# Kernel optimization log

Hardware: AMD Instinct MI355X
Metric: run time of the kernel (lower is better)

## Reference

```python
import jax, jax.numpy as jnp
import numpy as np

EMB, QK, V, H = 1024, 64, 64, 16
B, S = 4, 2048


def setup_inputs() -> dict:
    key = jax.random.key(0)
    ks = jax.random.split(key, 8)
    sc = 0.02
    x_q = jax.random.normal(ks[0], (B, S, EMB), jnp.float32)
    x_k_v = jax.random.normal(ks[1], (B, S, EMB), jnp.float32)
    # causal mask: True means masked (matches torch masked_fill)
    causal = ~jnp.tril(jnp.ones((S, S), dtype=bool))
    attn_mask = jnp.broadcast_to(causal, (B, S, S))
    w_q = jax.random.normal(ks[2], (H * QK, EMB), jnp.float32) * sc
    b_q = jnp.zeros((H * QK,), jnp.float32)
    w_k = jax.random.normal(ks[3], (H * QK, EMB), jnp.float32) * sc
    b_k = jnp.zeros((H * QK,), jnp.float32)
    w_v = jax.random.normal(ks[4], (H * V, EMB), jnp.float32) * sc
    b_v = jnp.zeros((H * V,), jnp.float32)
    return {"x_q": x_q, "x_k_v": x_k_v, "attn_mask": attn_mask,
            "w_q": w_q, "b_q": b_q, "w_k": w_k, "b_k": b_k, "w_v": w_v, "b_v": b_v}


def reference(x_q, x_k_v, attn_mask, w_q, b_q, w_k, b_k, w_v, b_v):
    Bq, Sq, _ = x_q.shape
    Skv = x_k_v.shape[1]
    q = (x_q @ w_q.T + b_q).reshape(Bq, Sq, H, QK).transpose(0, 2, 1, 3)   # [B,H,Sq,QK]
    k = (x_k_v @ w_k.T + b_k).reshape(Bq, Skv, H, QK).transpose(0, 2, 1, 3)  # [B,H,Skv,QK]
    v = (x_k_v @ w_v.T + b_v).reshape(Bq, Skv, H, V).transpose(0, 2, 1, 3)   # [B,H,Skv,V]
    attn = jnp.einsum('bhqd,bhkd->bhqk', q, k) / jnp.sqrt(jnp.float32(QK))
    attn = jnp.where(attn_mask[:, None, :, :], jnp.float32(-1e9), attn)
    attn = jax.nn.softmax(attn, axis=-1)
    z = jnp.einsum('bhqk,bhkv->bhqv', attn, v)        # [B,H,Sq,V]
    z = z.transpose(0, 2, 1, 3).reshape(Bq, Sq, H * V)
    return z
```

## Files before the change

### kernel.cpp

```cpp
#include <hip/hip_runtime.h>

#define B_    4
#define H_    16
#define S_    2048
#define EMB_  1024
#define D_    64

typedef __attribute__((ext_vector_type(4))) float f32x4;
typedef __attribute__((ext_vector_type(8))) short frag_ab;
typedef unsigned short ushort_t;

__device__ __forceinline__ unsigned short f2bf(float f) {
    unsigned int u = __float_as_uint(f);
    unsigned int r = u + 0x7fffu + ((u >> 16) & 1u);
    return (unsigned short)(r >> 16);
}
__device__ __forceinline__ unsigned short f2bf_fast(float f) {
    return (unsigned short)((__float_as_uint(f) + 0x8000u) >> 16);
}

__device__ __forceinline__ void gld16(const void* g, void* l) {
    __builtin_amdgcn_global_load_lds(
        (const __attribute__((address_space(1))) void*)g,
        (__attribute__((address_space(3))) void*)l, 16, 0, 0);
}

__global__ void cvt3_kernel(const float* __restrict__ s0, const float* __restrict__ s1,
                            const float* __restrict__ s2, ushort_t* __restrict__ d0,
                            ushort_t* __restrict__ d1, ushort_t* __restrict__ d2, int n4) {
    const float* src = (blockIdx.z == 0) ? s0 : (blockIdx.z == 1 ? s1 : s2);
    ushort_t* dst = (blockIdx.z == 0) ? d0 : (blockIdx.z == 1 ? d1 : d2);
    int i = blockIdx.x * blockDim.x + threadIdx.x;
    if (i >= n4) return;
    float4 f = ((const float4*)src)[i];
    ushort4 o;
    o.x = f2bf(f.x); o.y = f2bf(f.y); o.z = f2bf(f.z); o.w = f2bf(f.w);
    ((ushort4*)dst)[i] = o;
}
__global__ void cvt2_kernel(const float* __restrict__ s0, const float* __restrict__ s1,
                            ushort_t* __restrict__ d0, ushort_t* __restrict__ d1, int n4) {
    const float* src = (blockIdx.z == 0) ? s0 : s1;
    ushort_t* dst = (blockIdx.z == 0) ? d0 : d1;
    int i = blockIdx.x * blockDim.x + threadIdx.x;
    if (i >= n4) return;
    float4 f = ((const float4*)src)[i];
    ushort4 o;
    o.x = f2bf(f.x); o.y = f2bf(f.y); o.z = f2bf(f.z); o.w = f2bf(f.w);
    ((ushort4*)dst)[i] = o;
}

__global__ __launch_bounds__(256) void vtrans_kernel(
    const ushort_t* __restrict__ v, ushort_t* __restrict__ vt) {
    const int bh = blockIdx.y;
    const int s0 = blockIdx.x * 32 + (threadIdx.x >> 6) * 8;
    const int d  = threadIdx.x & 63;
    const ushort_t* vp = v + (size_t)bh * S_ * D_;
    ushort_t tmp[8];
#pragma unroll
    for (int j = 0; j < 8; ++j) tmp[j] = vp[(size_t)(s0 + j) * D_ + d];
    *(uint4*)&vt[(size_t)bh * D_ * S_ + (size_t)d * S_ + s0] = *(const uint4*)tmp;
}

__global__ __launch_bounds__(256) void qkv_gemm(
    const ushort_t* __restrict__ xq,
    const ushort_t* __restrict__ xkv,
    const ushort_t* __restrict__ wq,
    const ushort_t* __restrict__ wk,
    const ushort_t* __restrict__ wv,
    const float* __restrict__ bq,
    const float* __restrict__ bk,
    const float* __restrict__ bv,
    ushort_t* __restrict__ qo,
    ushort_t* __restrict__ ko,
    ushort_t* __restrict__ vo)
{
    __shared__ ushort_t As[2][128 * 32];
    __shared__ ushort_t Bs[2][128 * 32];

    const int z = blockIdx.z;
    const ushort_t* A = (z == 0) ? xq : xkv;
    const ushort_t* W = (z == 0) ? wq : (z == 1 ? wk : wv);
    const float* bias = (z == 0) ? bq : (z == 1 ? bk : bv);
    ushort_t* ob = (z == 0) ? qo : (z == 1 ? ko : vo);
    const float scale = (z == 0) ? 0.125f : 1.0f;

    const int tid = threadIdx.x;
    const int m0 = blockIdx.y * 128, n0 = blockIdx.x * 128;
    const int w = tid >> 6, lane = tid & 63, quad = lane >> 4, l16 = lane & 15;
    const int wm = w & 1, wn = w >> 1;
    const int row_in = lane >> 2, c8 = (lane & 3) * 8;

    f32x4 acc[4][4];
#pragma unroll
    for (int i = 0; i < 4; ++i)
#pragma unroll
        for (int j = 0; j < 4; ++j) acc[i][j] = (f32x4){0.f, 0.f, 0.f, 0.f};

    auto stage = [&](int b, int kt) {
        const int k0 = kt * 32;
#pragma unroll
        for (int i = 0; i < 2; ++i) {
            const int base = w * 32 + i * 16;
            gld16(A + (size_t)(m0 + base + row_in) * EMB_ + k0 + c8, &As[b][base * 32]);
            gld16(W + (size_t)(n0 + base + row_in) * EMB_ + k0 + c8, &Bs[b][base * 32]);
        }
    };

    stage(0, 0);
    for (int kt = 0; kt < 32; ++kt) {
        __syncthreads();
        if (kt < 31) stage((kt + 1) & 1, kt + 1);
        const int bsel = kt & 1;

        frag_ab a[4], bfr[4];
#pragma unroll
        for (int t = 0; t < 4; ++t) {
            a[t]   = *(const frag_ab*)&As[bsel][(wm * 64 + t * 16 + l16) * 32 + quad * 8];
            bfr[t] = *(const frag_ab*)&Bs[bsel][(wn * 64 + t * 16 + l16) * 32 + quad * 8];
        }
#pragma unroll
        for (int tm = 0; tm < 4; ++tm)
#pragma unroll
            for (int tn = 0; tn < 4; ++tn)
                acc[tm][tn] = __builtin_amdgcn_mfma_f32_16x16x32_bf16(
                    a[tm], bfr[tn], acc[tm][tn], 0, 0, 0);
    }

#pragma unroll
    for (int tn = 0; tn < 4; ++tn) {
        int n = n0 + wn * 64 + tn * 16 + l16;
        float bval = bias[n];
        int hh = n >> 6, dd = n & 63;
#pragma unroll
        for (int tm = 0; tm < 4; ++tm) {
#pragma unroll
            for (int r = 0; r < 4; ++r) {
                int m = m0 + wm * 64 + tm * 16 + quad * 4 + r;
                int bb = m >> 11, ss = m & (S_ - 1);
                float val = (acc[tm][tn][r] + bval) * scale;
                ob[(((size_t)bb * H_ + hh) * S_ + ss) * D_ + dd] = f2bf(val);
            }
        }
    }
}

#define LDP 72

__global__ __launch_bounds__(256) void attn_kernel(
    const ushort_t* __restrict__ qg,
    const ushort_t* __restrict__ kg,
    const ushort_t* __restrict__ vtg,
    float* __restrict__ out)
{
    __shared__ ushort_t Kt[2][2][64 * 32];
    __shared__ ushort_t Vt[2][2][64 * 32];
    __shared__ ushort_t Pb[4][32 * LDP];

    const int tid = threadIdx.x;
    const int w = tid >> 6, lane = tid & 63, quad = lane >> 4, l16 = lane & 15;
    const int row_in = lane >> 2, c8 = (lane & 3) * 8;

    const int id = blockIdx.x;
    const int rr = id >> 3;
    const int bh = (id & 7) + 8 * (rr & 7);
    const int qi = 15 - (rr >> 3);
    const int q0 = qi * 128;
    const int b = bh >> 4, h = bh & 15;

    const ushort_t* qp  = qg  + (size_t)bh * S_ * D_;
    const ushort_t* kp  = kg  + (size_t)bh * S_ * D_;
    const ushort_t* vtp = vtg + (size_t)bh * D_ * S_;

    frag_ab aq[2][2];
#pragma unroll
    for (int rg = 0; rg < 2; ++rg) {
        const ushort_t* qr = qp + (size_t)(q0 + rg * 64 + w * 16 + l16) * D_;
        aq[rg][0] = *(const frag_ab*)(qr + quad * 8);
        aq[rg][1] = *(const frag_ab*)(qr + 32 + quad * 8);
    }

    float psum[2][4];
    f32x4 o[2][4];
#pragma unroll
    for (int rg = 0; rg < 2; ++rg)
#pragma unroll
        for (int r = 0; r < 4; ++r) { psum[rg][r] = 0.f; }
#pragma unroll
    for (int rg = 0; rg < 2; ++rg)
#pragma unroll
        for (int t = 0; t < 4; ++t) o[rg][t] = (f32x4){0.f, 0.f, 0.f, 0.f};

    ushort_t* Pw = &Pb[w][0];
    const int last = 2 * qi + 1;

    auto stage = [&](int bsel, int kt) {
        const int base = w * 16;
        const ushort_t* kgp  = kp  + (size_t)(kt * 64 + base + row_in) * D_ + c8;
        const ushort_t* vtgp = vtp + (size_t)(base + row_in) * S_ + kt * 64 + c8;
        gld16(kgp,       &Kt[bsel][0][base * 32]);
        gld16(kgp + 32,  &Kt[bsel][1][base * 32]);
        gld16(vtgp,      &Vt[bsel][0][base * 32]);
        gld16(vtgp + 32, &Vt[bsel][1][base * 32]);
    };

    stage(0, 0);
    for (int kt = 0; kt <= last; ++kt) {
        __syncthreads();
        if (kt < last) stage((kt + 1) & 1, kt + 1);
        const int bsel = kt & 1;

        frag_ab bk[4][2], bv[4][2];
#pragma unroll
        for (int t = 0; t < 4; ++t) {
#pragma unroll
            for (int hf = 0; hf < 2; ++hf) {
                bk[t][hf] = *(const frag_ab*)&Kt[bsel][hf][(t * 16 + l16) * 32 + quad * 8];
                bv[t][hf] = *(const frag_ab*)&Vt[bsel][hf][(t * 16 + l16) * 32 + quad * 8];
            }
        }

#pragma unroll
        for (int rg = 0; rg < 2; ++rg) {
            if (rg == 0 && kt == last) continue;
            f32x4 scf[4];
#pragma unroll
            for (int tn = 0; tn < 4; ++tn) {
                f32x4 sc = (f32x4){0.f, 0.f, 0.f, 0.f};
                sc = __builtin_amdgcn_mfma_f32_16x16x32_bf16(aq[rg][0], bk[tn][0], sc, 0, 0, 0);
                sc = __builtin_amdgcn_mfma_f32_16x16x32_bf16(aq[rg][1], bk[tn][1], sc, 0, 0, 0);
                scf[tn] = sc;
            }
            if (kt == 2 * qi + rg) {
#pragma unroll
                for (int tn = 0; tn < 4; ++tn) {
                    int kcol = kt * 64 + tn * 16 + l16;
#pragma unroll
                    for (int r = 0; r < 4; ++r) {
                        int qrow = q0 + rg * 64 + w * 16 + quad * 4 + r;
                        if (kcol > qrow) scf[tn][r] = -1e30f;
                    }
                }
            }
#pragma unroll
            for (int tn = 0; tn < 4; ++tn) {
#pragma unroll
                for (int r = 0; r < 4; ++r) {
                    float p = __expf(scf[tn][r]);
                    psum[rg][r] += p;
                    Pw[(rg * 16 + quad * 4 + r) * LDP + tn * 16 + l16] = f2bf_fast(p);
                }
            }
        }
        asm volatile("s_waitcnt lgkmcnt(0)" ::: "memory");
#pragma unroll
        for (int rg = 0; rg < 2; ++rg) {
            if (rg == 0 && kt == last) continue;
            frag_ab ap0 = *(const frag_ab*)&Pw[(rg * 16 + l16) * LDP + quad * 8];
            frag_ab ap1 = *(const frag_ab*)&Pw[(rg * 16 + l16) * LDP + 32 + quad * 8];
#pragma unroll
            for (int tv = 0; tv < 4; ++tv) {
                o[rg][tv] = __builtin_amdgcn_mfma_f32_16x16x32_bf16(ap0, bv[tv][0], o[rg][tv], 0, 0, 0);
                o[rg][tv] = __builtin_amdgcn_mfma_f32_16x16x32_bf16(ap1, bv[tv][1], o[rg][tv], 0, 0, 0);
            }
        }
    }

    float* ob = out + (size_t)b * S_ * (H_ * D_) + h * D_;
#pragma unroll
    for (int rg = 0; rg < 2; ++rg) {
#pragma unroll
        for (int r = 0; r < 4; ++r) {
            float s = psum[rg][r];
            s += __shfl_xor(s, 1);
            s += __shfl_xor(s, 2);
            s += __shfl_xor(s, 4);
            s += __shfl_xor(s, 8);
            float inv = 1.0f / s;
            int srow = q0 + rg * 64 + w * 16 + quad * 4 + r;
#pragma unroll
            for (int tv = 0; tv < 4; ++tv)
                ob[(size_t)srow * (H_ * D_) + tv * 16 + l16] = o[rg][tv][r] * inv;
        }
    }
}

extern "C" void kernel_launch(void* const* d_in, const int* in_sizes, int n_in,
                              void* d_out, int out_size, void* d_ws, size_t ws_size,
                              hipStream_t stream) {
    const float* x_q  = (const float*)d_in[0];
    const float* x_kv = (const float*)d_in[1];
    const float* w_q  = (const float*)d_in[3];
    const float* b_q  = (const float*)d_in[4];
    const float* w_k  = (const float*)d_in[5];
    const float* b_k  = (const float*)d_in[6];
    const float* w_v  = (const float*)d_in[7];
    const float* b_v  = (const float*)d_in[8];
    float* out = (float*)d_out;

    ushort_t* ws  = (ushort_t*)d_ws;
    ushort_t* wqb = ws;
    ushort_t* wkb = wqb + 1048576;
    ushort_t* wvb = wkb + 1048576;
    ushort_t* xqb  = wvb + 1048576;
    ushort_t* xkvb = xqb + 8388608;
    ushort_t* qb   = xkvb + 8388608;
    ushort_t* kb   = qb + 8388608;
    ushort_t* vb   = kb + 8388608;
    ushort_t* vtb  = vb + 8388608;

    cvt3_kernel<<<dim3(1024, 1, 3), 256, 0, stream>>>(
        w_q, w_k, w_v, wqb, wkb, wvb, 262144);
    cvt2_kernel<<<dim3(8192, 1, 2), 256, 0, stream>>>(
        x_q, x_kv, xqb, xkvb, 2097152);
    qkv_gemm<<<dim3(8, 64, 3), 256, 0, stream>>>(
        xqb, xkvb, wqb, wkb, wvb, b_q, b_k, b_v, qb, kb, vb);
    vtrans_kernel<<<dim3(64, 64), 256, 0, stream>>>(vb, vtb);
    attn_kernel<<<1024, 256, 0, stream>>>(qb, kb, vtb, out);
}
```

Baseline: 321.4 us.

## Compute transposed scores to keep P in registers and remap GEMM blocks per XCD

The attention kernel now computes S^T (K as the A operand, Q as the B operand), so each lane holds probabilities laid out to feed the PV MFMA directly as bf16x4 fragments through the 16x16x16 bf16 instruction. This removes the per-wave LDS round trip for P, its s_waitcnt, and the scattered scalar stores. It also simplifies the row-sum reduction and allows vectorized f32x4 output stores. Separately, the QKV GEMM switches to a 1D grid with an XCD-aware tile mapping and precomputed load pointers, meant to improve L2 locality. The cost is more, smaller MFMAs and V fragment loads issued per tv inside the loop.

```diff
diff --git a/kernel.cpp b/kernel.cpp
--- a/kernel.cpp
+++ b/kernel.cpp
@@ -8,6 +8,7 @@
 
 typedef __attribute__((ext_vector_type(4))) float f32x4;
 typedef __attribute__((ext_vector_type(8))) short frag_ab;
+typedef __attribute__((ext_vector_type(4))) short bf16x4;
 typedef unsigned short ushort_t;
 
 __device__ __forceinline__ unsigned short f2bf(float f) {
@@ -77,7 +78,12 @@
     __shared__ ushort_t As[2][128 * 32];
     __shared__ ushort_t Bs[2][128 * 32];
 
-    const int z = blockIdx.z;
+    const int id = blockIdx.x;
+    const int xcd = id & 7, j = id >> 3;
+    const int m_t = xcd * 8 + (j & 7);
+    const int n_t = (j >> 3) & 7;
+    const int z   = j >> 6;
+
     const ushort_t* A = (z == 0) ? xq : xkv;
     const ushort_t* W = (z == 0) ? wq : (z == 1 ? wk : wv);
     const float* bias = (z == 0) ? bq : (z == 1 ? bk : bv);
@@ -85,7 +91,7 @@
     const float scale = (z == 0) ? 0.125f : 1.0f;
 
     const int tid = threadIdx.x;
-    const int m0 = blockIdx.y * 128, n0 = blockIdx.x * 128;
+    const int m0 = m_t * 128, n0 = n_t * 128;
     const int w = tid >> 6, lane = tid & 63, quad = lane >> 4, l16 = lane & 15;
     const int wm = w & 1, wn = w >> 1;
     const int row_in = lane >> 2, c8 = (lane & 3) * 8;
@@ -94,16 +100,18 @@
 #pragma unroll
     for (int i = 0; i < 4; ++i)
 #pragma unroll
-        for (int j = 0; j < 4; ++j) acc[i][j] = (f32x4){0.f, 0.f, 0.f, 0.f};
-
-    auto stage = [&](int b, int kt) {
+        for (int j2 = 0; j2 < 4; ++j2) acc[i][j2] = (f32x4){0.f, 0.f, 0.f, 0.f};
+
+    const ushort_t* pa = A + (size_t)(m0 + w * 32 + row_in) * EMB_ + c8;
+    const ushort_t* pw = W + (size_t)(n0 + w * 32 + row_in) * EMB_ + c8;
+
+    auto stage = [&](int bsel, int kt) {
         const int k0 = kt * 32;
-#pragma unroll
-        for (int i = 0; i < 2; ++i) {
-            const int base = w * 32 + i * 16;
-            gld16(A + (size_t)(m0 + base + row_in) * EMB_ + k0 + c8, &As[b][base * 32]);
-            gld16(W + (size_t)(n0 + base + row_in) * EMB_ + k0 + c8, &Bs[b][base * 32]);
-        }
+        const int base = w * 32;
+        gld16(pa + k0,             &As[bsel][base * 32]);
+        gld16(pa + 16 * EMB_ + k0, &As[bsel][(base + 16) * 32]);
+        gld16(pw + k0,             &Bs[bsel][base * 32]);
+        gld16(pw + 16 * EMB_ + k0, &Bs[bsel][(base + 16) * 32]);
     };
 
     stage(0, 0);
@@ -143,8 +151,6 @@
         }
     }
 }
-
-#define LDP 72
 
 __global__ __launch_bounds__(256) void attn_kernel(
     const ushort_t* __restrict__ qg,
@@ -154,7 +160,6 @@
 {
     __shared__ ushort_t Kt[2][2][64 * 32];
     __shared__ ushort_t Vt[2][2][64 * 32];
-    __shared__ ushort_t Pb[4][32 * LDP];
 
     const int tid = threadIdx.x;
     const int w = tid >> 6, lane = tid & 63, quad = lane >> 4, l16 = lane & 15;
@@ -172,25 +177,22 @@
     const ushort_t* vtp = vtg + (size_t)bh * D_ * S_;
 
     frag_ab aq[2][2];
+    int qrow[2];
 #pragma unroll
     for (int rg = 0; rg < 2; ++rg) {
-        const ushort_t* qr = qp + (size_t)(q0 + rg * 64 + w * 16 + l16) * D_;
+        qrow[rg] = q0 + rg * 64 + w * 16 + l16;
+        const ushort_t* qr = qp + (size_t)qrow[rg] * D_;
         aq[rg][0] = *(const frag_ab*)(qr + quad * 8);
         aq[rg][1] = *(const frag_ab*)(qr + 32 + quad * 8);
     }
 
-    float psum[2][4];
+    float psum[2] = {0.f, 0.f};
     f32x4 o[2][4];
 #pragma unroll
     for (int rg = 0; rg < 2; ++rg)
 #pragma unroll
-        for (int r = 0; r < 4; ++r) { psum[rg][r] = 0.f; }
-#pragma unroll
-    for (int rg = 0; rg < 2; ++rg)
-#pragma unroll
         for (int t = 0; t < 4; ++t) o[rg][t] = (f32x4){0.f, 0.f, 0.f, 0.f};
 
-    ushort_t* Pw = &Pb[w][0];
     const int last = 2 * qi + 1;
 
     auto stage = [&](int bsel, int kt) {
@@ -209,77 +211,69 @@
         if (kt < last) stage((kt + 1) & 1, kt + 1);
         const int bsel = kt & 1;
 
-        frag_ab bk[4][2], bv[4][2];
+        frag_ab ak[4][2];
 #pragma unroll
         for (int t = 0; t < 4; ++t) {
-#pragma unroll
-            for (int hf = 0; hf < 2; ++hf) {
-                bk[t][hf] = *(const frag_ab*)&Kt[bsel][hf][(t * 16 + l16) * 32 + quad * 8];
-                bv[t][hf] = *(const frag_ab*)&Vt[bsel][hf][(t * 16 + l16) * 32 + quad * 8];
-            }
-        }
-
+            ak[t][0] = *(const frag_ab*)&Kt[bsel][0][(t * 16 + l16) * 32 + quad * 8];
+            ak[t][1] = *(const frag_ab*)&Kt[bsel][1][(t * 16 + l16) * 32 + quad * 8];
+        }
+
+        bf16x4 pp[2][4];
 #pragma unroll
         for (int rg = 0; rg < 2; ++rg) {
             if (rg == 0 && kt == last) continue;
-            f32x4 scf[4];
+            const bool diag = (kt == 2 * qi + rg);
 #pragma unroll
             for (int tn = 0; tn < 4; ++tn) {
                 f32x4 sc = (f32x4){0.f, 0.f, 0.f, 0.f};
-                sc = __builtin_amdgcn_mfma_f32_16x16x32_bf16(aq[rg][0], bk[tn][0], sc, 0, 0, 0);
-                sc = __builtin_amdgcn_mfma_f32_16x16x32_bf16(aq[rg][1], bk[tn][1], sc, 0, 0, 0);
-                scf[tn] = sc;
+                sc = __builtin_amdgcn_mfma_f32_16x16x32_bf16(ak[tn][0], aq[rg][0], sc, 0, 0, 0);
+                sc = __builtin_amdgcn_mfma_f32_16x16x32_bf16(ak[tn][1], aq[rg][1], sc, 0, 0, 0);
+                union { bf16x4 v; ushort_t u[4]; } pk;
+#pragma unroll
+                for (int r = 0; r < 4; ++r) {
+                    float p = __expf(sc[r]);
+                    if (diag) {
+                        int s_idx = kt * 64 + tn * 16 + quad * 4 + r;
+                        if (s_idx > qrow[rg]) p = 0.f;
+                    }
+                    psum[rg] += p;
+                    pk.u[r] = f2bf_fast(p);
+                }
+                pp[rg][tn] = pk.v;
             }
-            if (kt == 2 * qi + rg) {
-#pragma unroll
-                for (int tn = 0; tn < 4; ++tn) {
-                    int kcol = kt * 64 + tn * 16 + l16;
-#pragma unroll
-                    for (int r = 0; r < 4; ++r) {
-                        int qrow = q0 + rg * 64 + w * 16 + quad * 4 + r;
-                        if (kcol > qrow) scf[tn][r] = -1e30f;
-                    }
-                }
+        }
+
+#pragma unroll
+        for (int tv = 0; tv < 4; ++tv) {
+            bf16x4 av[4];
+#pragma unroll
+            for (int si = 0; si < 4; ++si)
+                av[si] = *(const bf16x4*)&Vt[bsel][si >> 1]
+                    [(tv * 16 + l16) * 32 + (si & 1) * 16 + quad * 4];
+#pragma unroll
+            for (int rg = 0; rg < 2; ++rg) {
+                if (rg == 0 && kt == last) continue;
+#pragma unroll
+                for (int si = 0; si < 4; ++si)
+                    o[rg][tv] = __builtin_amdgcn_mfma_f32_16x16x16bf16_1k(
+                        av[si], pp[rg][si], o[rg][tv], 0, 0, 0);
             }
-#pragma unroll
-            for (int tn = 0; tn < 4; ++tn) {
-#pragma unroll
-                for (int r = 0; r < 4; ++r) {
-                    float p = __expf(scf[tn][r]);
-                    psum[rg][r] += p;
-                    Pw[(rg * 16 + quad * 4 + r) * LDP + tn * 16 + l16] = f2bf_fast(p);
-                }
-            }
-        }
-        asm volatile("s_waitcnt lgkmcnt(0)" ::: "memory");
-#pragma unroll
-        for (int rg = 0; rg < 2; ++rg) {
-            if (rg == 0 && kt == last) continue;
-            frag_ab ap0 = *(const frag_ab*)&Pw[(rg * 16 + l16) * LDP + quad * 8];
-            frag_ab ap1 = *(const frag_ab*)&Pw[(rg * 16 + l16) * LDP + 32 + quad * 8];
-#pragma unroll
-            for (int tv = 0; tv < 4; ++tv) {
-                o[rg][tv] = __builtin_amdgcn_mfma_f32_16x16x32_bf16(ap0, bv[tv][0], o[rg][tv], 0, 0, 0);
-                o[rg][tv] = __builtin_amdgcn_mfma_f32_16x16x32_bf16(ap1, bv[tv][1], o[rg][tv], 0, 0, 0);
-            }
-        }
-    }
-
-    float* ob = out + (size_t)b * S_ * (H_ * D_) + h * D_;
+        }
+    }
+
+    float* ob = out + ((size_t)b * S_) * (H_ * D_) + h * D_;
 #pragma unroll
     for (int rg = 0; rg < 2; ++rg) {
-#pragma unroll
-        for (int r = 0; r < 4; ++r) {
-            float s = psum[rg][r];
-            s += __shfl_xor(s, 1);
-            s += __shfl_xor(s, 2);
-            s += __shfl_xor(s, 4);
-            s += __shfl_xor(s, 8);
-            float inv = 1.0f / s;
-            int srow = q0 + rg * 64 + w * 16 + quad * 4 + r;
-#pragma unroll
-            for (int tv = 0; tv < 4; ++tv)
-                ob[(size_t)srow * (H_ * D_) + tv * 16 + l16] = o[rg][tv][r] * inv;
+        float s = psum[rg];
+        s += __shfl_xor(s, 16);
+        s += __shfl_xor(s, 32);
+        float inv = 1.0f / s;
+        float* obr = ob + (size_t)qrow[rg] * (H_ * D_);
+#pragma unroll
+        for (int tv = 0; tv < 4; ++tv) {
+            f32x4 val = o[rg][tv];
+            val[0] *= inv; val[1] *= inv; val[2] *= inv; val[3] *= inv;
+            *(f32x4*)&obr[tv * 16 + quad * 4] = val;
         }
     }
 }
@@ -312,7 +306,7 @@
         w_q, w_k, w_v, wqb, wkb, wvb, 262144);
     cvt2_kernel<<<dim3(8192, 1, 2), 256, 0, stream>>>(
         x_q, x_kv, xqb, xkvb, 2097152);
-    qkv_gemm<<<dim3(8, 64, 3), 256, 0, stream>>>(
+    qkv_gemm<<<1536, 256, 0, stream>>>(
         xqb, xkvb, wqb, wkb, wvb, b_q, b_k, b_v, qb, kb, vb);
     vtrans_kernel<<<dim3(64, 64), 256, 0, stream>>>(vb, vtb);
     attn_kernel<<<1024, 256, 0, stream>>>(qb, kb, vtb, out);
```

Measured after the change: 345.1 us. 1.07x slower.
